# Optimization experiments

Measured on AMD Instinct MI355X. Metric: run time of the kernel, lower is better.

The kernel has to match this reference:

```python
import jax, jax.numpy as jnp
import numpy as np

N = 50000       # nodes
E = 600000      # edges
F_IN = 500      # num_feature
H = 64          # hidden_dim (ODE state = 2*H)
C = 40          # num_class
T = 1.0         # integration time
STEPS = 4       # RK4 steps (16 ODE function evals)


def setup_inputs() -> dict:
    key = jax.random.key(0)
    ks = jax.random.split(key, 7)
    x = jax.random.normal(ks[0], (N, F_IN), dtype=jnp.float32)
    edge_src = jax.random.randint(ks[1], (E,), 0, N, dtype=jnp.int32)
    edge_dst = jax.random.randint(ks[2], (E,), 0, N, dtype=jnp.int32)
    edge_w = jax.random.uniform(ks[3], (E,), dtype=jnp.float32)
    m1_w = jax.random.normal(ks[4], (F_IN, H), dtype=jnp.float32) / np.sqrt(F_IN).astype(np.float32)
    m1_b = jnp.zeros((H,), jnp.float32)
    alpha_train = jnp.ones((N,), jnp.float32)  # alpha * ones(N) with alpha=1.0
    m2_w = jax.random.normal(ks[5], (H, C), dtype=jnp.float32) / np.sqrt(H).astype(np.float32)
    m2_b = jnp.zeros((C,), jnp.float32)
    return dict(x=x, edge_w=edge_w, m1_w=m1_w, m1_b=m1_b,
                alpha_train=alpha_train, m2_w=m2_w, m2_b=m2_b,
                edge_src=edge_src, edge_dst=edge_dst)


def spmm(edge_src, edge_dst, edge_w, z):
    # A @ z where A[i,j] = sum of edge_w over edges (src=i, dst=j)
    msg = edge_w[:, None] * z[edge_dst]           # [E, 2H]
    return jax.ops.segment_sum(msg, edge_src, num_segments=N)


def reference(x, edge_w, m1_w, m1_b, alpha_train, m2_w, m2_b, edge_src, edge_dst):
    # Encoder (dropout is identity in eval mode)
    h = x @ m1_w + m1_b                           # [N, H]
    h = jnp.concatenate([h, jnp.zeros_like(h)], axis=1)  # [N, 2H]
    x0 = jax.lax.stop_gradient(h)                 # x0 = x.clone().detach()
    alph = jax.nn.sigmoid(alpha_train)[:, None]   # [N, 1]

    def f(z):  # ODE RHS: sigmoid(alpha)*0.5*(A z - z) + x0
        az = spmm(edge_src, edge_dst, edge_w, z)
        return alph * 0.5 * (az - z) + x0

    dt = jnp.float32(T / STEPS)

    def step(z, _):
        k1 = f(z)
        k2 = f(z + 0.5 * dt * k1)
        k3 = f(z + 0.5 * dt * k2)
        k4 = f(z + dt * k3)
        return z + (dt / 6.0) * (k1 + 2.0 * k2 + 2.0 * k3 + k4), None

    z, _ = jax.lax.scan(step, h, None, length=STEPS)
    z = jax.nn.relu(z[:, :H])                     # first half of state
    return z @ m2_w + m2_b                        # [N, C]
```

## Files before the change

### kernel.cpp

```cpp
#include <hip/hip_runtime.h>
#include <hip/hip_fp16.h>

#define N_NODES 50000
#define N_EDGES 600000
#define F_IN    500
#define H_DIM   64
#define C_OUT   40
#define STEPS   4
#define NB_SCAN ((N_NODES + 255) / 256)
#define KTILES  16

using half8 = __attribute__((ext_vector_type(8))) _Float16;
using f32x4 = __attribute__((ext_vector_type(4))) float;

__global__ __launch_bounds__(256) void bfrag_kernel(
    const float* __restrict__ W, __half* __restrict__ bfrag)
{
    int t = blockIdx.x * 256 + threadIdx.x;
    if (t >= KTILES * 4 * 64) return;
    int lane = t & 63;
    int c    = (t >> 6) & 3;
    int kt   = t >> 8;
    int col  = c * 16 + (lane & 15);
    int kb   = kt * 32 + (lane >> 4) * 8;
    union { uint4 u; __half h[8]; } v;
    #pragma unroll
    for (int j = 0; j < 8; ++j) {
        int k = kb + j;
        v.h[j] = (k < F_IN) ? __float2half(W[(size_t)k * H_DIM + col]) : __half(0.f);
    }
    *reinterpret_cast<uint4*>(bfrag + (size_t)t * 8) = v.u;
}

__global__ __launch_bounds__(256) void encoder_kernel(
    const float* __restrict__ x, const __half* __restrict__ bfrag,
    const float* __restrict__ b, __half* __restrict__ x0H,
    float* __restrict__ zF, __half* __restrict__ zH)
{
    __shared__ f32x4 red[2][64][4];

    int wave = threadIdx.x >> 6;
    int lane = threadIdx.x & 63;
    int pair = wave >> 1;
    int half = wave & 1;
    int rowl = lane & 15;
    int kg   = lane >> 4;
    int r0   = blockIdx.x * 32 + pair * 16;

    int gr = r0 + rowl; if (gr >= N_NODES) gr = N_NODES - 1;
    const float* xrow = x + (size_t)gr * F_IN;
    const uint4* bf = reinterpret_cast<const uint4*>(bfrag);

    int ktb = half * 8;

    float4 xv[16];
    #pragma unroll
    for (int ki = 0; ki < 8; ++ki) {
        int k0 = (ktb + ki) * 32 + kg * 8;
        xv[2 * ki]     = make_float4(0.f, 0.f, 0.f, 0.f);
        xv[2 * ki + 1] = make_float4(0.f, 0.f, 0.f, 0.f);
        if (k0 + 4 <= F_IN) xv[2 * ki]     = *reinterpret_cast<const float4*>(xrow + k0);
        if (k0 + 8 <= F_IN) xv[2 * ki + 1] = *reinterpret_cast<const float4*>(xrow + k0 + 4);
    }

    f32x4 acc[4];
    #pragma unroll
    for (int c = 0; c < 4; ++c) acc[c] = (f32x4){0.f, 0.f, 0.f, 0.f};

    #pragma unroll
    for (int ki = 0; ki < 8; ++ki) {
        int kt = ktb + ki;
        float4 xa = xv[2 * ki], xb = xv[2 * ki + 1];
        half8 a;
        a[0] = (_Float16)xa.x; a[1] = (_Float16)xa.y;
        a[2] = (_Float16)xa.z; a[3] = (_Float16)xa.w;
        a[4] = (_Float16)xb.x; a[5] = (_Float16)xb.y;
        a[6] = (_Float16)xb.z; a[7] = (_Float16)xb.w;
        #pragma unroll
        for (int c = 0; c < 4; ++c) {
            union { uint4 u; half8 h; } bv;
            bv.u = bf[(size_t)(kt * 4 + c) * 64 + lane];
            acc[c] = __builtin_amdgcn_mfma_f32_16x16x32_f16(a, bv.h, acc[c], 0, 0, 0);
        }
    }

    if (half == 1) {
        #pragma unroll
        for (int c = 0; c < 4; ++c) red[pair][lane][c] = acc[c];
    }
    __syncthreads();
    if (half == 0) {
        #pragma unroll
        for (int c = 0; c < 4; ++c) {
            f32x4 r = red[pair][lane][c];
            acc[c][0] += r[0]; acc[c][1] += r[1];
            acc[c][2] += r[2]; acc[c][3] += r[3];
        }
        #pragma unroll
        for (int c = 0; c < 4; ++c) {
            int col = c * 16 + rowl;
            float bias = b[col];
            #pragma unroll
            for (int r = 0; r < 4; ++r) {
                int grow = r0 + kg * 4 + r;
                if (grow < N_NODES) {
                    float v = acc[c][r] + bias;
                    size_t idx = (size_t)grow * H_DIM + col;
                    zF[idx]  = v;
                    __half hv = __float2half(v);
                    zH[idx]  = hv;
                    x0H[idx] = hv;
                }
            }
        }
    }
}

__global__ void hist_kernel(const int* __restrict__ src, int* __restrict__ counts)
{
    int e = blockIdx.x * 256 + threadIdx.x;
    if (e < N_EDGES) atomicAdd(&counts[src[e]], 1);
}

__global__ __launch_bounds__(256) void scanA_kernel(
    const int* __restrict__ counts, int* __restrict__ blockSums)
{
    __shared__ int red[256];
    int i = blockIdx.x * 256 + threadIdx.x;
    red[threadIdx.x] = (i < N_NODES) ? counts[i] : 0;
    __syncthreads();
    #pragma unroll
    for (int s = 128; s > 0; s >>= 1) {
        if (threadIdx.x < s) red[threadIdx.x] += red[threadIdx.x + s];
        __syncthreads();
    }
    if (threadIdx.x == 0) blockSums[blockIdx.x] = red[0];
}

__global__ __launch_bounds__(256) void scanB_kernel(
    const int* __restrict__ blockSums, int* __restrict__ blockBases)
{
    __shared__ int s[256];
    int tid = threadIdx.x;
    int v = (tid < NB_SCAN) ? blockSums[tid] : 0;
    s[tid] = v;
    __syncthreads();
    #pragma unroll
    for (int d = 1; d < 256; d <<= 1) {
        int t = (tid >= d) ? s[tid - d] : 0;
        __syncthreads();
        s[tid] += t;
        __syncthreads();
    }
    if (tid < NB_SCAN) blockBases[tid] = s[tid] - v;
}

__global__ __launch_bounds__(256) void scanC_kernel(
    const int* __restrict__ counts, const int* __restrict__ blockBases,
    int* __restrict__ off, int* __restrict__ cursor)
{
    __shared__ int s[256];
    int tid = threadIdx.x;
    int i = blockIdx.x * 256 + tid;
    int v = (i < N_NODES) ? counts[i] : 0;
    s[tid] = v;
    __syncthreads();
    #pragma unroll
    for (int d = 1; d < 256; d <<= 1) {
        int t = (tid >= d) ? s[tid - d] : 0;
        __syncthreads();
        s[tid] += t;
        __syncthreads();
    }
    if (i < N_NODES) {
        int excl = blockBases[blockIdx.x] + s[tid] - v;
        off[i] = excl;
        cursor[i] = excl;
        if (i == N_NODES - 1) off[N_NODES] = excl + v;
    }
}

__global__ void scatter_kernel(const int* __restrict__ src, const int* __restrict__ dst,
                               const float* __restrict__ w,
                               int* __restrict__ cursor, int2* __restrict__ epack)
{
    int e = blockIdx.x * 256 + threadIdx.x;
    if (e < N_EDGES) {
        int s = src[e];
        int p = atomicAdd(&cursor[s], 1);
        epack[p] = make_int2(dst[e], __float_as_int(w[e]));
    }
}

template<int STAGE>
__global__ __launch_bounds__(256) void stage_kernel(
    const int* __restrict__ off, const int2* __restrict__ epack,
    const __half* __restrict__ zsH, const __half* __restrict__ zH,
    const float* __restrict__ zbF, const __half* __restrict__ x0H,
    const float* __restrict__ alpha, __half* __restrict__ accH,
    __half* __restrict__ outH, float* __restrict__ outZ, float cnext)
{
    int node = blockIdx.x * 32 + (threadIdx.x >> 3);
    if (node >= N_NODES) return;
    int c = (threadIdx.x & 7) << 3;

    int jb = off[node], je = off[node + 1];

    union H4 { uint4 u; __half2 h[4]; };

    float azA[8], azB[8];
    #pragma unroll
    for (int i = 0; i < 8; ++i) { azA[i] = 0.f; azB[i] = 0.f; }

#define ACC8(dst, V, W)                                                    \
    {                                                                      \
        float2 f0 = __half22float2((V).h[0]);                              \
        float2 f1 = __half22float2((V).h[1]);                              \
        float2 f2 = __half22float2((V).h[2]);                              \
        float2 f3 = __half22float2((V).h[3]);                              \
        dst[0] = fmaf(W, f0.x, dst[0]); dst[1] = fmaf(W, f0.y, dst[1]);    \
        dst[2] = fmaf(W, f1.x, dst[2]); dst[3] = fmaf(W, f1.y, dst[3]);    \
        dst[4] = fmaf(W, f2.x, dst[4]); dst[5] = fmaf(W, f2.y, dst[5]);    \
        dst[6] = fmaf(W, f3.x, dst[6]); dst[7] = fmaf(W, f3.y, dst[7]);    \
    }

    int j = jb;
    for (; j + 3 < je; j += 4) {
        int2 e0 = epack[j];
        int2 e1 = epack[j + 1];
        int2 e2 = epack[j + 2];
        int2 e3 = epack[j + 3];
        H4 v0, v1, v2, v3;
        v0.u = *reinterpret_cast<const uint4*>(zsH + (size_t)e0.x * H_DIM + c);
        v1.u = *reinterpret_cast<const uint4*>(zsH + (size_t)e1.x * H_DIM + c);
        v2.u = *reinterpret_cast<const uint4*>(zsH + (size_t)e2.x * H_DIM + c);
        v3.u = *reinterpret_cast<const uint4*>(zsH + (size_t)e3.x * H_DIM + c);
        float w0 = __int_as_float(e0.y), w1 = __int_as_float(e1.y);
        float w2 = __int_as_float(e2.y), w3 = __int_as_float(e3.y);
        ACC8(azA, v0, w0);
        ACC8(azB, v1, w1);
        ACC8(azA, v2, w2);
        ACC8(azB, v3, w3);
    }
    for (; j < je; ++j) {
        int2 e0 = epack[j];
        H4 v0;
        v0.u = *reinterpret_cast<const uint4*>(zsH + (size_t)e0.x * H_DIM + c);
        float w0 = __int_as_float(e0.y);
        ACC8(azA, v0, w0);
    }
#undef ACC8

    float az[8];
    #pragma unroll
    for (int i = 0; i < 8; ++i) az[i] = azA[i] + azB[i];

    size_t idx = (size_t)node * H_DIM + c;
    H4 sr; sr.u = *reinterpret_cast<const uint4*>(zsH + idx);
    float s[8];
    {
        float2 f0 = __half22float2(sr.h[0]), f1 = __half22float2(sr.h[1]);
        float2 f2 = __half22float2(sr.h[2]), f3 = __half22float2(sr.h[3]);
        s[0] = f0.x; s[1] = f0.y; s[2] = f1.x; s[3] = f1.y;
        s[4] = f2.x; s[5] = f2.y; s[6] = f3.x; s[7] = f3.y;
    }
    H4 xr; xr.u = *reinterpret_cast<const uint4*>(x0H + idx);
    float xv[8];
    {
        float2 f0 = __half22float2(xr.h[0]), f1 = __half22float2(xr.h[1]);
        float2 f2 = __half22float2(xr.h[2]), f3 = __half22float2(xr.h[3]);
        xv[0] = f0.x; xv[1] = f0.y; xv[2] = f1.x; xv[3] = f1.y;
        xv[4] = f2.x; xv[5] = f2.y; xv[6] = f3.x; xv[7] = f3.y;
    }
    float a = 0.5f / (1.f + __expf(-alpha[node]));

    float k[8];
    #pragma unroll
    for (int i = 0; i < 8; ++i) k[i] = fmaf(a, az[i] - s[i], xv[i]);

    float o[8];
    if constexpr (STAGE == 0) {
        H4 aw;
        aw.h[0] = __float22half2_rn(make_float2(k[0], k[1]));
        aw.h[1] = __float22half2_rn(make_float2(k[2], k[3]));
        aw.h[2] = __float22half2_rn(make_float2(k[4], k[5]));
        aw.h[3] = __float22half2_rn(make_float2(k[6], k[7]));
        *reinterpret_cast<uint4*>(accH + idx) = aw.u;
        #pragma unroll
        for (int i = 0; i < 8; ++i) o[i] = fmaf(cnext, k[i], s[i]);
    } else if constexpr (STAGE == 1 || STAGE == 2) {
        H4 ar; ar.u = *reinterpret_cast<const uint4*>(accH + idx);
        float av[8];
        {
            float2 f0 = __half22float2(ar.h[0]), f1 = __half22float2(ar.h[1]);
            float2 f2 = __half22float2(ar.h[2]), f3 = __half22float2(ar.h[3]);
            av[0] = f0.x; av[1] = f0.y; av[2] = f1.x; av[3] = f1.y;
            av[4] = f2.x; av[5] = f2.y; av[6] = f3.x; av[7] = f3.y;
        }
        #pragma unroll
        for (int i = 0; i < 8; ++i) av[i] = fmaf(2.f, k[i], av[i]);
        H4 aw;
        aw.h[0] = __float22half2_rn(make_float2(av[0], av[1]));
        aw.h[1] = __float22half2_rn(make_float2(av[2], av[3]));
        aw.h[2] = __float22half2_rn(make_float2(av[4], av[5]));
        aw.h[3] = __float22half2_rn(make_float2(av[6], av[7]));
        *reinterpret_cast<uint4*>(accH + idx) = aw.u;
        H4 br; br.u = *reinterpret_cast<const uint4*>(zH + idx);
        float bv[8];
        {
            float2 f0 = __half22float2(br.h[0]), f1 = __half22float2(br.h[1]);
            float2 f2 = __half22float2(br.h[2]), f3 = __half22float2(br.h[3]);
            bv[0] = f0.x; bv[1] = f0.y; bv[2] = f1.x; bv[3] = f1.y;
            bv[4] = f2.x; bv[5] = f2.y; bv[6] = f3.x; bv[7] = f3.y;
        }
        #pragma unroll
        for (int i = 0; i < 8; ++i) o[i] = fmaf(cnext, k[i], bv[i]);
    } else {
        H4 ar; ar.u = *reinterpret_cast<const uint4*>(accH + idx);
        float av[8];
        {
            float2 f0 = __half22float2(ar.h[0]), f1 = __half22float2(ar.h[1]);
            float2 f2 = __half22float2(ar.h[2]), f3 = __half22float2(ar.h[3]);
            av[0] = f0.x; av[1] = f0.y; av[2] = f1.x; av[3] = f1.y;
            av[4] = f2.x; av[5] = f2.y; av[6] = f3.x; av[7] = f3.y;
        }
        float4 zb0 = *reinterpret_cast<const float4*>(zbF + idx);
        float4 zb1 = *reinterpret_cast<const float4*>(zbF + idx + 4);
        float zb[8] = {zb0.x, zb0.y, zb0.z, zb0.w, zb1.x, zb1.y, zb1.z, zb1.w};
        #pragma unroll
        for (int i = 0; i < 8; ++i) o[i] = fmaf(cnext, av[i] + k[i], zb[i]);
        float4 oz0 = make_float4(o[0], o[1], o[2], o[3]);
        float4 oz1 = make_float4(o[4], o[5], o[6], o[7]);
        *reinterpret_cast<float4*>(outZ + idx)     = oz0;
        *reinterpret_cast<float4*>(outZ + idx + 4) = oz1;
    }
    H4 sv;
    sv.h[0] = __float22half2_rn(make_float2(o[0], o[1]));
    sv.h[1] = __float22half2_rn(make_float2(o[2], o[3]));
    sv.h[2] = __float22half2_rn(make_float2(o[4], o[5]));
    sv.h[3] = __float22half2_rn(make_float2(o[6], o[7]));
    *reinterpret_cast<uint4*>(outH + idx) = sv.u;
}

__global__ __launch_bounds__(256) void decoder_kernel(
    const float* __restrict__ z, const float* __restrict__ W2,
    const float* __restrict__ b2, float* __restrict__ out)
{
    __shared__ float zsm[4][H_DIM];
    int lane = threadIdx.x & 63;
    int w    = threadIdx.x >> 6;
    int node = blockIdx.x * 4 + w;
    int ld   = node >= N_NODES ? N_NODES - 1 : node;
    float zv = z[(size_t)ld * H_DIM + lane];
    zsm[w][lane] = zv > 0.f ? zv : 0.f;
    __syncthreads();
    if (node < N_NODES && lane < C_OUT) {
        float acc = b2[lane];
        #pragma unroll
        for (int k = 0; k < H_DIM; ++k)
            acc = fmaf(zsm[w][k], W2[k * C_OUT + lane], acc);
        out[(size_t)node * C_OUT + lane] = acc;
    }
}

extern "C" void kernel_launch(void* const* d_in, const int* in_sizes, int n_in,
                              void* d_out, int out_size, void* d_ws, size_t ws_size,
                              hipStream_t stream)
{
    const float* x     = (const float*)d_in[0];
    const float* ew    = (const float*)d_in[1];
    const float* m1w   = (const float*)d_in[2];
    const float* m1b   = (const float*)d_in[3];
    const float* alpha = (const float*)d_in[4];
    const float* m2w   = (const float*)d_in[5];
    const float* m2b   = (const float*)d_in[6];
    const int*   esrc  = (const int*)d_in[7];
    const int*   edst  = (const int*)d_in[8];
    float* out = (float*)d_out;

    char* ws = (char*)d_ws;
    size_t o = 0;
    auto alloc = [&](size_t bytes) -> void* {
        void* p = ws + o;
        o = (o + bytes + 255) & ~(size_t)255;
        return p;
    };
    float*  z      = (float*)alloc((size_t)N_NODES * H_DIM * 4);
    __half* x0H    = (__half*)alloc((size_t)N_NODES * H_DIM * 2);
    __half* zH     = (__half*)alloc((size_t)N_NODES * H_DIM * 2);
    __half* ztAH   = (__half*)alloc((size_t)N_NODES * H_DIM * 2);
    __half* ztBH   = (__half*)alloc((size_t)N_NODES * H_DIM * 2);
    __half* accH   = (__half*)alloc((size_t)N_NODES * H_DIM * 2);
    __half* bfrag  = (__half*)alloc((size_t)KTILES * 4 * 64 * 8 * 2);
    int*    counts = (int*)alloc((size_t)N_NODES * 4);
    int*    off    = (int*)alloc((size_t)(N_NODES + 1) * 4);
    int*    cursor = (int*)alloc((size_t)N_NODES * 4);
    int*    bsums  = (int*)alloc((size_t)NB_SCAN * 4);
    int*    bbases = (int*)alloc((size_t)NB_SCAN * 4);
    int2*   epack  = (int2*)alloc((size_t)N_EDGES * 8);

    hipMemsetAsync(counts, 0, (size_t)N_NODES * 4, stream);
    hist_kernel<<<(N_EDGES + 255) / 256, 256, 0, stream>>>(esrc, counts);
    scanA_kernel<<<NB_SCAN, 256, 0, stream>>>(counts, bsums);
    scanB_kernel<<<1, 256, 0, stream>>>(bsums, bbases);
    scanC_kernel<<<NB_SCAN, 256, 0, stream>>>(counts, bbases, off, cursor);
    scatter_kernel<<<(N_EDGES + 255) / 256, 256, 0, stream>>>(esrc, edst, ew, cursor, epack);

    bfrag_kernel<<<(KTILES * 4 * 64 + 255) / 256, 256, 0, stream>>>(m1w, bfrag);
    encoder_kernel<<<(N_NODES + 31) / 32, 256, 0, stream>>>(x, bfrag, m1b, x0H, z, zH);

    const float dt = 1.0f / STEPS;
    int sgrid = (N_NODES + 31) / 32;
    for (int step = 0; step < STEPS; ++step) {
        stage_kernel<0><<<sgrid, 256, 0, stream>>>(off, epack, zH,   zH, nullptr, x0H, alpha, accH, ztAH, nullptr, 0.5f * dt);
        stage_kernel<1><<<sgrid, 256, 0, stream>>>(off, epack, ztAH, zH, nullptr, x0H, alpha, accH, ztBH, nullptr, 0.5f * dt);
        stage_kernel<2><<<sgrid, 256, 0, stream>>>(off, epack, ztBH, zH, nullptr, x0H, alpha, accH, ztAH, nullptr, dt);
        stage_kernel<3><<<sgrid, 256, 0, stream>>>(off, epack, ztAH, zH, z,       x0H, alpha, accH, zH,   z,       dt / 6.0f);
    }

    decoder_kernel<<<(N_NODES + 3) / 4, 256, 0, stream>>>(z, m2w, m2b, out);
}
```

Measured before the change: 393.7 us.

## Drop fp32 ODE state, prescale gather indices, and split encoder K over four waves

The fp32 copy of the ODE state is removed, so the RK4 final stage reads its base from the fp16 zH and the decoder reads fp16. This cuts the fp32 read and write traffic per step. Edge destinations are stored pre-shifted to byte offsets (dst<<7) so the gather skips the index multiply. The encoder now uses 16 rows per block with four waves each doing a quarter of K and reducing through shared memory. Keeping the state only in fp16 accumulates rounding error across the RK4 steps.

```diff
diff --git a/kernel.cpp b/kernel.cpp
--- a/kernel.cpp
+++ b/kernel.cpp
@@ -35,27 +35,25 @@
 __global__ __launch_bounds__(256) void encoder_kernel(
     const float* __restrict__ x, const __half* __restrict__ bfrag,
     const float* __restrict__ b, __half* __restrict__ x0H,
-    float* __restrict__ zF, __half* __restrict__ zH)
-{
-    __shared__ f32x4 red[2][64][4];
+    __half* __restrict__ zH)
+{
+    __shared__ f32x4 red[3][64][4];
 
     int wave = threadIdx.x >> 6;
     int lane = threadIdx.x & 63;
-    int pair = wave >> 1;
-    int half = wave & 1;
     int rowl = lane & 15;
     int kg   = lane >> 4;
-    int r0   = blockIdx.x * 32 + pair * 16;
+    int r0   = blockIdx.x * 16;
 
     int gr = r0 + rowl; if (gr >= N_NODES) gr = N_NODES - 1;
     const float* xrow = x + (size_t)gr * F_IN;
     const uint4* bf = reinterpret_cast<const uint4*>(bfrag);
 
-    int ktb = half * 8;
-
-    float4 xv[16];
-    #pragma unroll
-    for (int ki = 0; ki < 8; ++ki) {
+    int ktb = wave * 4;
+
+    float4 xv[8];
+    #pragma unroll
+    for (int ki = 0; ki < 4; ++ki) {
         int k0 = (ktb + ki) * 32 + kg * 8;
         xv[2 * ki]     = make_float4(0.f, 0.f, 0.f, 0.f);
         xv[2 * ki + 1] = make_float4(0.f, 0.f, 0.f, 0.f);
@@ -68,7 +66,7 @@
     for (int c = 0; c < 4; ++c) acc[c] = (f32x4){0.f, 0.f, 0.f, 0.f};
 
     #pragma unroll
-    for (int ki = 0; ki < 8; ++ki) {
+    for (int ki = 0; ki < 4; ++ki) {
         int kt = ktb + ki;
         float4 xa = xv[2 * ki], xb = xv[2 * ki + 1];
         half8 a;
@@ -84,18 +82,20 @@
         }
     }
 
-    if (half == 1) {
-        #pragma unroll
-        for (int c = 0; c < 4; ++c) red[pair][lane][c] = acc[c];
+    if (wave > 0) {
+        #pragma unroll
+        for (int c = 0; c < 4; ++c) red[wave - 1][lane][c] = acc[c];
     }
     __syncthreads();
-    if (half == 0) {
-        #pragma unroll
-        for (int c = 0; c < 4; ++c) {
-            f32x4 r = red[pair][lane][c];
-            acc[c][0] += r[0]; acc[c][1] += r[1];
-            acc[c][2] += r[2]; acc[c][3] += r[3];
-        }
+    if (wave == 0) {
+        #pragma unroll
+        for (int w = 0; w < 3; ++w)
+            #pragma unroll
+            for (int c = 0; c < 4; ++c) {
+                f32x4 r = red[w][lane][c];
+                acc[c][0] += r[0]; acc[c][1] += r[1];
+                acc[c][2] += r[2]; acc[c][3] += r[3];
+            }
         #pragma unroll
         for (int c = 0; c < 4; ++c) {
             int col = c * 16 + rowl;
@@ -106,7 +106,6 @@
                 if (grow < N_NODES) {
                     float v = acc[c][r] + bias;
                     size_t idx = (size_t)grow * H_DIM + col;
-                    zF[idx]  = v;
                     __half hv = __float2half(v);
                     zH[idx]  = hv;
                     x0H[idx] = hv;
@@ -188,7 +187,7 @@
     if (e < N_EDGES) {
         int s = src[e];
         int p = atomicAdd(&cursor[s], 1);
-        epack[p] = make_int2(dst[e], __float_as_int(w[e]));
+        epack[p] = make_int2(dst[e] << 7, __float_as_int(w[e]));
     }
 }
 
@@ -196,15 +195,16 @@
 __global__ __launch_bounds__(256) void stage_kernel(
     const int* __restrict__ off, const int2* __restrict__ epack,
     const __half* __restrict__ zsH, const __half* __restrict__ zH,
-    const float* __restrict__ zbF, const __half* __restrict__ x0H,
-    const float* __restrict__ alpha, __half* __restrict__ accH,
-    __half* __restrict__ outH, float* __restrict__ outZ, float cnext)
+    const __half* __restrict__ x0H, const float* __restrict__ alpha,
+    __half* __restrict__ accH, __half* __restrict__ outH, float cnext)
 {
     int node = blockIdx.x * 32 + (threadIdx.x >> 3);
     if (node >= N_NODES) return;
-    int c = (threadIdx.x & 7) << 3;
+    int cb = (threadIdx.x & 7) << 4;
+    int c  = cb >> 1;
 
     int jb = off[node], je = off[node + 1];
+    const char* rdB = reinterpret_cast<const char*>(zsH);
 
     union H4 { uint4 u; __half2 h[4]; };
 
@@ -231,10 +231,10 @@
         int2 e2 = epack[j + 2];
         int2 e3 = epack[j + 3];
         H4 v0, v1, v2, v3;
-        v0.u = *reinterpret_cast<const uint4*>(zsH + (size_t)e0.x * H_DIM + c);
-        v1.u = *reinterpret_cast<const uint4*>(zsH + (size_t)e1.x * H_DIM + c);
-        v2.u = *reinterpret_cast<const uint4*>(zsH + (size_t)e2.x * H_DIM + c);
-        v3.u = *reinterpret_cast<const uint4*>(zsH + (size_t)e3.x * H_DIM + c);
+        v0.u = *reinterpret_cast<const uint4*>(rdB + (size_t)(unsigned)e0.x + cb);
+        v1.u = *reinterpret_cast<const uint4*>(rdB + (size_t)(unsigned)e1.x + cb);
+        v2.u = *reinterpret_cast<const uint4*>(rdB + (size_t)(unsigned)e2.x + cb);
+        v3.u = *reinterpret_cast<const uint4*>(rdB + (size_t)(unsigned)e3.x + cb);
         float w0 = __int_as_float(e0.y), w1 = __int_as_float(e1.y);
         float w2 = __int_as_float(e2.y), w3 = __int_as_float(e3.y);
         ACC8(azA, v0, w0);
@@ -245,7 +245,7 @@
     for (; j < je; ++j) {
         int2 e0 = epack[j];
         H4 v0;
-        v0.u = *reinterpret_cast<const uint4*>(zsH + (size_t)e0.x * H_DIM + c);
+        v0.u = *reinterpret_cast<const uint4*>(rdB + (size_t)(unsigned)e0.x + cb);
         float w0 = __int_as_float(e0.y);
         ACC8(azA, v0, w0);
     }
@@ -324,15 +324,16 @@
             av[0] = f0.x; av[1] = f0.y; av[2] = f1.x; av[3] = f1.y;
             av[4] = f2.x; av[5] = f2.y; av[6] = f3.x; av[7] = f3.y;
         }
-        float4 zb0 = *reinterpret_cast<const float4*>(zbF + idx);
-        float4 zb1 = *reinterpret_cast<const float4*>(zbF + idx + 4);
-        float zb[8] = {zb0.x, zb0.y, zb0.z, zb0.w, zb1.x, zb1.y, zb1.z, zb1.w};
-        #pragma unroll
-        for (int i = 0; i < 8; ++i) o[i] = fmaf(cnext, av[i] + k[i], zb[i]);
-        float4 oz0 = make_float4(o[0], o[1], o[2], o[3]);
-        float4 oz1 = make_float4(o[4], o[5], o[6], o[7]);
-        *reinterpret_cast<float4*>(outZ + idx)     = oz0;
-        *reinterpret_cast<float4*>(outZ + idx + 4) = oz1;
+        H4 br; br.u = *reinterpret_cast<const uint4*>(zH + idx);
+        float bv[8];
+        {
+            float2 f0 = __half22float2(br.h[0]), f1 = __half22float2(br.h[1]);
+            float2 f2 = __half22float2(br.h[2]), f3 = __half22float2(br.h[3]);
+            bv[0] = f0.x; bv[1] = f0.y; bv[2] = f1.x; bv[3] = f1.y;
+            bv[4] = f2.x; bv[5] = f2.y; bv[6] = f3.x; bv[7] = f3.y;
+        }
+        #pragma unroll
+        for (int i = 0; i < 8; ++i) o[i] = fmaf(cnext, av[i] + k[i], bv[i]);
     }
     H4 sv;
     sv.h[0] = __float22half2_rn(make_float2(o[0], o[1]));
@@ -343,7 +344,7 @@
 }
 
 __global__ __launch_bounds__(256) void decoder_kernel(
-    const float* __restrict__ z, const float* __restrict__ W2,
+    const __half* __restrict__ zH, const float* __restrict__ W2,
     const float* __restrict__ b2, float* __restrict__ out)
 {
     __shared__ float zsm[4][H_DIM];
@@ -351,7 +352,7 @@
     int w    = threadIdx.x >> 6;
     int node = blockIdx.x * 4 + w;
     int ld   = node >= N_NODES ? N_NODES - 1 : node;
-    float zv = z[(size_t)ld * H_DIM + lane];
+    float zv = __half2float(zH[(size_t)ld * H_DIM + lane]);
     zsm[w][lane] = zv > 0.f ? zv : 0.f;
     __syncthreads();
     if (node < N_NODES && lane < C_OUT) {
@@ -385,7 +386,6 @@
         o = (o + bytes + 255) & ~(size_t)255;
         return p;
     };
-    float*  z      = (float*)alloc((size_t)N_NODES * H_DIM * 4);
     __half* x0H    = (__half*)alloc((size_t)N_NODES * H_DIM * 2);
     __half* zH     = (__half*)alloc((size_t)N_NODES * H_DIM * 2);
     __half* ztAH   = (__half*)alloc((size_t)N_NODES * H_DIM * 2);
@@ -407,16 +407,16 @@
     scatter_kernel<<<(N_EDGES + 255) / 256, 256, 0, stream>>>(esrc, edst, ew, cursor, epack);
 
     bfrag_kernel<<<(KTILES * 4 * 64 + 255) / 256, 256, 0, stream>>>(m1w, bfrag);
-    encoder_kernel<<<(N_NODES + 31) / 32, 256, 0, stream>>>(x, bfrag, m1b, x0H, z, zH);
+    encoder_kernel<<<(N_NODES + 15) / 16, 256, 0, stream>>>(x, bfrag, m1b, x0H, zH);
 
     const float dt = 1.0f / STEPS;
     int sgrid = (N_NODES + 31) / 32;
     for (int step = 0; step < STEPS; ++step) {
-        stage_kernel<0><<<sgrid, 256, 0, stream>>>(off, epack, zH,   zH, nullptr, x0H, alpha, accH, ztAH, nullptr, 0.5f * dt);
-        stage_kernel<1><<<sgrid, 256, 0, stream>>>(off, epack, ztAH, zH, nullptr, x0H, alpha, accH, ztBH, nullptr, 0.5f * dt);
-        stage_kernel<2><<<sgrid, 256, 0, stream>>>(off, epack, ztBH, zH, nullptr, x0H, alpha, accH, ztAH, nullptr, dt);
-        stage_kernel<3><<<sgrid, 256, 0, stream>>>(off, epack, ztAH, zH, z,       x0H, alpha, accH, zH,   z,       dt / 6.0f);
-    }
-
-    decoder_kernel<<<(N_NODES + 3) / 4, 256, 0, stream>>>(z, m2w, m2b, out);
-}
+        stage_kernel<0><<<sgrid, 256, 0, stream>>>(off, epack, zH,   zH, x0H, alpha, accH, ztAH, 0.5f * dt);
+        stage_kernel<1><<<sgrid, 256, 0, stream>>>(off, epack, ztAH, zH, x0H, alpha, accH, ztBH, 0.5f * dt);
+        stage_kernel<2><<<sgrid, 256, 0, stream>>>(off, epack, ztBH, zH, x0H, alpha, accH, ztAH, dt);
+        stage_kernel<3><<<sgrid, 256, 0, stream>>>(off, epack, ztAH, zH, x0H, alpha, accH, zH,   dt / 6.0f);
+    }
+
+    decoder_kernel<<<(N_NODES + 3) / 4, 256, 0, stream>>>(zH, m2w, m2b, out);
+}
```

Result: no change. 389.1 us (-1.2%).
